# Performance work log

Hardware: AMD Instinct MI355X
Metric: run time of the kernel (lower is better)

Reference implementation:

```python
import jax, jax.numpy as jnp
import numpy as np

B, L, D = 1, 512, 1280


def setup_inputs() -> dict:
    key = jax.random.key(0)
    k1, k2, k3 = jax.random.split(key, 3)
    prev_result = jax.random.normal(k1, (B, L, D), dtype=jnp.float32)
    # nn.Linear(2*D, 2): store weight as [2D, 2] so forward is x @ W + b
    W = jax.random.normal(k2, (2 * D, 2), dtype=jnp.float32) * (1.0 / np.sqrt(2 * D))
    b = jax.random.normal(k3, (2,), dtype=jnp.float32) * 0.01
    return {"prev_result": prev_result, "W": W, "b": b}


def reference(prev_result, W, b):
    # Dropout is identity at inference. The torch code builds
    # pairwise = cat(x_i * x_j, x_i - x_j) of shape [B,L,L,2D] then applies
    # Linear(2D, 2). We fuse: split W into the prod half Wp and diff half Wd.
    Wp, Wd = W[:D], W[D:]                                   # each [D, 2]
    # (x_i * x_j) @ Wp  -- bilinear contraction, no [B,L,L,2D] intermediate
    prod_term = jnp.einsum('bid,bjd,dk->bijk', prev_result, prev_result, Wp)
    # (x_i - x_j) @ Wd = (x @ Wd)_i - (x @ Wd)_j
    d_proj = prev_result @ Wd                                # [B, L, 2]
    diff_term = d_proj[:, :, None, :] - d_proj[:, None, :, :]
    prediction = prod_term + diff_term + b                   # [B, L, L, 2]
    prediction = (prediction + prediction.transpose(0, 2, 1, 3)) / 2
    return prediction[:, 1:-1, 1:-1]                         # [B, L-2, L-2, 2]
```

## Files before the change

### kernel.cpp

```cpp
#include <hip/hip_runtime.h>
#include <math.h>

#define D_DIM 1280
#define ODIM  510
#define KSTEPS 40
#define QK    320

typedef short bf16x8 __attribute__((ext_vector_type(8)));
typedef float f32x4  __attribute__((ext_vector_type(4)));

__device__ __forceinline__ unsigned pkbf(float a, float b) {
  unsigned ua = __float_as_uint(a), ub = __float_as_uint(b);
  return ((ua + 0x8000u) >> 16) | ((ub + 0x8000u) & 0xffff0000u);
}

__global__ __launch_bounds__(256, 1) void pcmd_prep(
    const float* __restrict__ X,
    const float* __restrict__ W,
    unsigned short* __restrict__ Xbf,
    unsigned short* __restrict__ A0,
    unsigned short* __restrict__ A1)
{
  __shared__ unsigned short sG[3][10][64][8];

  const int R   = (int)blockIdx.x >> 2;
  const int q   = (int)blockIdx.x & 3;
  const int tid = threadIdx.x;

  for (int task = tid; task < 640; task += 256) {
    const int lr = task / 40;
    const int gc = task - lr * 40;
    const int s = gc >> 2, quad = gc & 3;
    const int prow = R * 16 + lr;
    uint4 vx = {0,0,0,0}, v0 = {0,0,0,0}, v1 = {0,0,0,0};
    if (prow <= 510) {
      const float* px = X + (size_t)(prow + 1) * D_DIM + q * QK + gc * 8;
      float4 x0 = *(const float4*)px;
      float4 x1 = *(const float4*)(px + 4);
      const float* pw = W + 2 * (q * QK + gc * 8);
      float4 w0 = *(const float4*)(pw +  0);
      float4 w1 = *(const float4*)(pw +  4);
      float4 w2 = *(const float4*)(pw +  8);
      float4 w3 = *(const float4*)(pw + 12);
      vx.x = pkbf(x0.x, x0.y);            vx.y = pkbf(x0.z, x0.w);
      vx.z = pkbf(x1.x, x1.y);            vx.w = pkbf(x1.z, x1.w);
      v0.x = pkbf(x0.x*w0.x, x0.y*w0.z);  v0.y = pkbf(x0.z*w1.x, x0.w*w1.z);
      v0.z = pkbf(x1.x*w2.x, x1.y*w2.z);  v0.w = pkbf(x1.z*w3.x, x1.w*w3.z);
      v1.x = pkbf(x0.x*w0.y, x0.y*w0.w);  v1.y = pkbf(x0.z*w1.y, x0.w*w1.w);
      v1.z = pkbf(x1.x*w2.y, x1.y*w2.w);  v1.w = pkbf(x1.z*w3.y, x1.w*w3.w);
    }
    const int swzl = quad * 16 + ((lr + quad + 4 * s) & 15);
    *(uint4*)&sG[0][s][swzl][0] = vx;
    *(uint4*)&sG[1][s][swzl][0] = v0;
    *(uint4*)&sG[2][s][swzl][0] = v1;
  }
  __syncthreads();

  for (int g = tid; g < 640; g += 256) {
    const int s = g >> 6, l = g & 63;
    const int quad = l >> 4, m = l & 15;
    const int swzl = quad * 16 + ((m + quad + 4 * s) & 15);
    const size_t go = ((size_t)((R * KSTEPS + q * 10 + s) * 64) + l) * 8;
    *(uint4*)(Xbf + go) = *(const uint4*)&sG[0][s][swzl][0];
    *(uint4*)(A0  + go) = *(const uint4*)&sG[1][s][swzl][0];
    *(uint4*)(A1  + go) = *(const uint4*)&sG[2][s][swzl][0];
  }
}

__global__ __launch_bounds__(256, 2) void pcmd_gemm(
    const unsigned short* __restrict__ Xbf,
    const unsigned short* __restrict__ A0,
    const unsigned short* __restrict__ A1,
    const float* __restrict__ b,
    float* __restrict__ out)
{
  __shared__ float sR[4][2][16][17];

  const int t = (int)blockIdx.x;
  int bi = (int)((65.0 - sqrt(4225.0 - 8.0 * (double)t)) * 0.5);
  {
    int s0 = bi * 32 - (bi * (bi - 1)) / 2;
    if (t < s0) { --bi; }
    int s1 = (bi + 1) * 32 - ((bi + 1) * bi) / 2;
    if (t >= s1) { ++bi; }
  }
  const int start = bi * 32 - (bi * (bi - 1)) / 2;
  const int bj = bi + (t - start);

  const int tid  = threadIdx.x;
  const int lane = tid & 63;
  const int wv   = tid >> 6;

  const unsigned short* pa0 = A0  + ((size_t)(bi * KSTEPS + wv * 10) * 64 + lane) * 8;
  const unsigned short* pa1 = A1  + ((size_t)(bi * KSTEPS + wv * 10) * 64 + lane) * 8;
  const unsigned short* pb  = Xbf + ((size_t)(bj * KSTEPS + wv * 10) * 64 + lane) * 8;

  bf16x8 ra0[4], ra1[4], rb[4];
  #pragma unroll
  for (int s = 0; s < 4; ++s) {
    ra0[s] = *(const bf16x8*)(pa0 + s * 512);
    ra1[s] = *(const bf16x8*)(pa1 + s * 512);
    rb[s]  = *(const bf16x8*)(pb  + s * 512);
  }

  f32x4 acc0 = {0.f, 0.f, 0.f, 0.f};
  f32x4 acc1 = {0.f, 0.f, 0.f, 0.f};

  #pragma unroll
  for (int s = 0; s < 10; ++s) {
    const int cur = s & 3;
    bf16x8 a0 = ra0[cur], a1 = ra1[cur], bb = rb[cur];
    if (s + 4 < 10) {
      ra0[cur] = *(const bf16x8*)(pa0 + (s + 4) * 512);
      ra1[cur] = *(const bf16x8*)(pa1 + (s + 4) * 512);
      rb[cur]  = *(const bf16x8*)(pb  + (s + 4) * 512);
    }
    acc0 = __builtin_amdgcn_mfma_f32_16x16x32_bf16(a0, bb, acc0, 0, 0, 0);
    acc1 = __builtin_amdgcn_mfma_f32_16x16x32_bf16(a1, bb, acc1, 0, 0, 0);
  }

  const int m = lane & 15, quad = lane >> 4;
  #pragma unroll
  for (int r = 0; r < 4; ++r) {
    sR[wv][0][quad * 4 + r][m] = acc0[r];
    sR[wv][1][quad * 4 + r][m] = acc1[r];
  }
  __syncthreads();

  const float b0 = b[0], b1 = b[1];
  const int il = tid >> 4, jl = tid & 15;

  {
    const int oi = bi * 16 + il, oj = bj * 16 + jl;
    if (oi < ODIM && oj < ODIM) {
      float2 v;
      v.x = sR[0][0][il][jl] + sR[1][0][il][jl] + sR[2][0][il][jl] + sR[3][0][il][jl] + b0;
      v.y = sR[0][1][il][jl] + sR[1][1][il][jl] + sR[2][1][il][jl] + sR[3][1][il][jl] + b1;
      *(float2*)(out + ((size_t)oi * ODIM + oj) * 2) = v;
    }
  }
  if (bi != bj) {
    const int oi = bj * 16 + il, oj = bi * 16 + jl;
    if (oi < ODIM && oj < ODIM) {
      float2 v;
      v.x = sR[0][0][jl][il] + sR[1][0][jl][il] + sR[2][0][jl][il] + sR[3][0][jl][il] + b0;
      v.y = sR[0][1][jl][il] + sR[1][1][jl][il] + sR[2][1][jl][il] + sR[3][1][jl][il] + b1;
      *(float2*)(out + ((size_t)oi * ODIM + oj) * 2) = v;
    }
  }
}

extern "C" void kernel_launch(void* const* d_in, const int* in_sizes, int n_in,
                              void* d_out, int out_size, void* d_ws, size_t ws_size,
                              hipStream_t stream) {
  const float* X = (const float*)d_in[0];
  const float* W = (const float*)d_in[1];
  const float* b = (const float*)d_in[2];
  float* out = (float*)d_out;
  (void)in_sizes; (void)n_in; (void)out_size; (void)ws_size;

  const size_t PLANE = (size_t)512 * D_DIM;
  unsigned short* Xbf = (unsigned short*)d_ws;
  unsigned short* A0  = Xbf + PLANE;
  unsigned short* A1  = A0 + PLANE;

  hipLaunchKernelGGL(pcmd_prep, dim3(128), dim3(256), 0, stream, X, W, Xbf, A0, A1);
  hipLaunchKernelGGL(pcmd_gemm, dim3(528), dim3(256), 0, stream, Xbf, A0, A1, b, out);
}
```

Before: 70.73 us.

## Fuse bf16 conversion prep kernel into GEMM, reading fp32 X directly

Removes the separate prep kernel that converted X and X*W to bf16 into workspace, and instead has the GEMM kernel load fp32 rows of X and W directly, multiply and pack to bf16 in registers before each MFMA. This eliminates one kernel launch and the workspace write/read round trip. In exchange each tile re-reads fp32 data (twice the bytes of bf16), redoes the conversion for every tile pair, and the prefetch depth drops from 4 stages to 2.

Result: slower. 74.63 us (+5.5%).

```diff
diff --git a/kernel.cpp b/kernel.cpp
--- a/kernel.cpp
+++ b/kernel.cpp
@@ -3,8 +3,6 @@
 
 #define D_DIM 1280
 #define ODIM  510
-#define KSTEPS 40
-#define QK    320
 
 typedef short bf16x8 __attribute__((ext_vector_type(8)));
 typedef float f32x4  __attribute__((ext_vector_type(4)));
@@ -14,64 +12,12 @@
   return ((ua + 0x8000u) >> 16) | ((ub + 0x8000u) & 0xffff0000u);
 }
 
-__global__ __launch_bounds__(256, 1) void pcmd_prep(
+union B8 { unsigned u[4]; bf16x8 v; };
+
+__global__ __launch_bounds__(256, 2) void pcmd_fused(
     const float* __restrict__ X,
     const float* __restrict__ W,
-    unsigned short* __restrict__ Xbf,
-    unsigned short* __restrict__ A0,
-    unsigned short* __restrict__ A1)
-{
-  __shared__ unsigned short sG[3][10][64][8];
-
-  const int R   = (int)blockIdx.x >> 2;
-  const int q   = (int)blockIdx.x & 3;
-  const int tid = threadIdx.x;
-
-  for (int task = tid; task < 640; task += 256) {
-    const int lr = task / 40;
-    const int gc = task - lr * 40;
-    const int s = gc >> 2, quad = gc & 3;
-    const int prow = R * 16 + lr;
-    uint4 vx = {0,0,0,0}, v0 = {0,0,0,0}, v1 = {0,0,0,0};
-    if (prow <= 510) {
-      const float* px = X + (size_t)(prow + 1) * D_DIM + q * QK + gc * 8;
-      float4 x0 = *(const float4*)px;
-      float4 x1 = *(const float4*)(px + 4);
-      const float* pw = W + 2 * (q * QK + gc * 8);
-      float4 w0 = *(const float4*)(pw +  0);
-      float4 w1 = *(const float4*)(pw +  4);
-      float4 w2 = *(const float4*)(pw +  8);
-      float4 w3 = *(const float4*)(pw + 12);
-      vx.x = pkbf(x0.x, x0.y);            vx.y = pkbf(x0.z, x0.w);
-      vx.z = pkbf(x1.x, x1.y);            vx.w = pkbf(x1.z, x1.w);
-      v0.x = pkbf(x0.x*w0.x, x0.y*w0.z);  v0.y = pkbf(x0.z*w1.x, x0.w*w1.z);
-      v0.z = pkbf(x1.x*w2.x, x1.y*w2.z);  v0.w = pkbf(x1.z*w3.x, x1.w*w3.z);
-      v1.x = pkbf(x0.x*w0.y, x0.y*w0.w);  v1.y = pkbf(x0.z*w1.y, x0.w*w1.w);
-      v1.z = pkbf(x1.x*w2.y, x1.y*w2.w);  v1.w = pkbf(x1.z*w3.y, x1.w*w3.w);
-    }
-    const int swzl = quad * 16 + ((lr + quad + 4 * s) & 15);
-    *(uint4*)&sG[0][s][swzl][0] = vx;
-    *(uint4*)&sG[1][s][swzl][0] = v0;
-    *(uint4*)&sG[2][s][swzl][0] = v1;
-  }
-  __syncthreads();
-
-  for (int g = tid; g < 640; g += 256) {
-    const int s = g >> 6, l = g & 63;
-    const int quad = l >> 4, m = l & 15;
-    const int swzl = quad * 16 + ((m + quad + 4 * s) & 15);
-    const size_t go = ((size_t)((R * KSTEPS + q * 10 + s) * 64) + l) * 8;
-    *(uint4*)(Xbf + go) = *(const uint4*)&sG[0][s][swzl][0];
-    *(uint4*)(A0  + go) = *(const uint4*)&sG[1][s][swzl][0];
-    *(uint4*)(A1  + go) = *(const uint4*)&sG[2][s][swzl][0];
-  }
-}
-
-__global__ __launch_bounds__(256, 2) void pcmd_gemm(
-    const unsigned short* __restrict__ Xbf,
-    const unsigned short* __restrict__ A0,
-    const unsigned short* __restrict__ A1,
-    const float* __restrict__ b,
+    const float* __restrict__ bias,
     float* __restrict__ out)
 {
   __shared__ float sR[4][2][16][17];
@@ -90,36 +36,52 @@
   const int tid  = threadIdx.x;
   const int lane = tid & 63;
   const int wv   = tid >> 6;
+  const int m    = lane & 15;
+  const int quad = lane >> 4;
 
-  const unsigned short* pa0 = A0  + ((size_t)(bi * KSTEPS + wv * 10) * 64 + lane) * 8;
-  const unsigned short* pa1 = A1  + ((size_t)(bi * KSTEPS + wv * 10) * 64 + lane) * 8;
-  const unsigned short* pb  = Xbf + ((size_t)(bj * KSTEPS + wv * 10) * 64 + lane) * 8;
-
-  bf16x8 ra0[4], ra1[4], rb[4];
-  #pragma unroll
-  for (int s = 0; s < 4; ++s) {
-    ra0[s] = *(const bf16x8*)(pa0 + s * 512);
-    ra1[s] = *(const bf16x8*)(pa1 + s * 512);
-    rb[s]  = *(const bf16x8*)(pb  + s * 512);
-  }
+  const int rA = min(bi * 16 + m + 1, 511);
+  const int rB = min(bj * 16 + m + 1, 511);
+  const int kq = wv * 320 + quad * 8;
+  const float* __restrict__ pa = X + (size_t)rA * D_DIM + kq;
+  const float* __restrict__ pb = X + (size_t)rB * D_DIM + kq;
+  const float* __restrict__ pw = W + 2 * kq;
 
   f32x4 acc0 = {0.f, 0.f, 0.f, 0.f};
   f32x4 acc1 = {0.f, 0.f, 0.f, 0.f};
 
+  float4 xa0[2], xa1[2], xb0[2], xb1[2], w0[2], w1[2], w2[2], w3[2];
+
+  xa0[0] = *(const float4*)(pa + 0);   xa1[0] = *(const float4*)(pa + 4);
+  xb0[0] = *(const float4*)(pb + 0);   xb1[0] = *(const float4*)(pb + 4);
+  w0[0]  = *(const float4*)(pw + 0);   w1[0]  = *(const float4*)(pw + 4);
+  w2[0]  = *(const float4*)(pw + 8);   w3[0]  = *(const float4*)(pw + 12);
+
   #pragma unroll
   for (int s = 0; s < 10; ++s) {
-    const int cur = s & 3;
-    bf16x8 a0 = ra0[cur], a1 = ra1[cur], bb = rb[cur];
-    if (s + 4 < 10) {
-      ra0[cur] = *(const bf16x8*)(pa0 + (s + 4) * 512);
-      ra1[cur] = *(const bf16x8*)(pa1 + (s + 4) * 512);
-      rb[cur]  = *(const bf16x8*)(pb  + (s + 4) * 512);
+    const int cur = s & 1, nxt = cur ^ 1;
+    if (s < 9) {
+      const int o = (s + 1) * 32;
+      xa0[nxt] = *(const float4*)(pa + o);          xa1[nxt] = *(const float4*)(pa + o + 4);
+      xb0[nxt] = *(const float4*)(pb + o);          xb1[nxt] = *(const float4*)(pb + o + 4);
+      w0[nxt]  = *(const float4*)(pw + 2 * o);      w1[nxt]  = *(const float4*)(pw + 2 * o + 4);
+      w2[nxt]  = *(const float4*)(pw + 2 * o + 8);  w3[nxt]  = *(const float4*)(pw + 2 * o + 12);
     }
-    acc0 = __builtin_amdgcn_mfma_f32_16x16x32_bf16(a0, bb, acc0, 0, 0, 0);
-    acc1 = __builtin_amdgcn_mfma_f32_16x16x32_bf16(a1, bb, acc1, 0, 0, 0);
+    const float4 xA0 = xa0[cur], xA1 = xa1[cur];
+    const float4 xB0 = xb0[cur], xB1 = xb1[cur];
+    const float4 W0 = w0[cur], W1 = w1[cur], W2 = w2[cur], W3 = w3[cur];
+
+    B8 fb, fa0, fa1;
+    fb.u[0] = pkbf(xB0.x, xB0.y);  fb.u[1] = pkbf(xB0.z, xB0.w);
+    fb.u[2] = pkbf(xB1.x, xB1.y);  fb.u[3] = pkbf(xB1.z, xB1.w);
+    fa0.u[0] = pkbf(xA0.x * W0.x, xA0.y * W0.z);  fa0.u[1] = pkbf(xA0.z * W1.x, xA0.w * W1.z);
+    fa0.u[2] = pkbf(xA1.x * W2.x, xA1.y * W2.z);  fa0.u[3] = pkbf(xA1.z * W3.x, xA1.w * W3.z);
+    fa1.u[0] = pkbf(xA0.x * W0.y, xA0.y * W0.w);  fa1.u[1] = pkbf(xA0.z * W1.y, xA0.w * W1.w);
+    fa1.u[2] = pkbf(xA1.x * W2.y, xA1.y * W2.w);  fa1.u[3] = pkbf(xA1.z * W3.y, xA1.w * W3.w);
+
+    acc0 = __builtin_amdgcn_mfma_f32_16x16x32_bf16(fa0.v, fb.v, acc0, 0, 0, 0);
+    acc1 = __builtin_amdgcn_mfma_f32_16x16x32_bf16(fa1.v, fb.v, acc1, 0, 0, 0);
   }
 
-  const int m = lane & 15, quad = lane >> 4;
   #pragma unroll
   for (int r = 0; r < 4; ++r) {
     sR[wv][0][quad * 4 + r][m] = acc0[r];
@@ -127,7 +89,7 @@
   }
   __syncthreads();
 
-  const float b0 = b[0], b1 = b[1];
+  const float b0 = bias[0], b1 = bias[1];
   const int il = tid >> 4, jl = tid & 15;
 
   {
@@ -157,13 +119,7 @@
   const float* W = (const float*)d_in[1];
   const float* b = (const float*)d_in[2];
   float* out = (float*)d_out;
-  (void)in_sizes; (void)n_in; (void)out_size; (void)ws_size;
+  (void)in_sizes; (void)n_in; (void)out_size; (void)d_ws; (void)ws_size;
 
-  const size_t PLANE = (size_t)512 * D_DIM;
-  unsigned short* Xbf = (unsigned short*)d_ws;
-  unsigned short* A0  = Xbf + PLANE;
-  unsigned short* A1  = A0 + PLANE;
-
-  hipLaunchKernelGGL(pcmd_prep, dim3(128), dim3(256), 0, stream, X, W, Xbf, A0, A1);
-  hipLaunchKernelGGL(pcmd_gemm, dim3(528), dim3(256), 0, stream, Xbf, A0, A1, b, out);
+  hipLaunchKernelGGL(pcmd_fused, dim3(528), dim3(256), 0, stream, X, W, b, out);
 }
```
